# Performance work log

Hardware: AMD Instinct MI355X
Metric: run time of the kernel (lower is better)

## Reference

```python
import jax, jax.numpy as jnp
import numpy as np
from jax import lax

B, T = 64, 512
VOCAB, E = 16000, 128
USCRIPT, UE = 64, 16
F, MAX_NGRAM = 128, 5
C = 13  # num_classes


def setup_inputs() -> dict:
    key = jax.random.key(0)
    ks = jax.random.split(key, 18)
    inp = {
        "input_char": jax.random.randint(ks[0], (B, T), 0, VOCAB),
        "input_script": jax.random.randint(ks[1], (B, T), 0, USCRIPT),
        "input_mask": jnp.ones((B, T), dtype=bool),
        "char_emb": jax.random.normal(ks[2], (VOCAB, E), jnp.float32) * 0.02,
        "uscript_emb": jax.random.normal(ks[3], (USCRIPT, UE), jnp.float32) * 0.02,
        "dense_w": jax.random.normal(ks[4], (MAX_NGRAM * F + UE, C), jnp.float32) * 0.05,
        "dense_b": jnp.zeros((C,), jnp.float32),
        "trans": jax.random.normal(ks[5], (C, C), jnp.float32) * 0.1,
        "left_b": jax.random.normal(ks[6], (C,), jnp.float32) * 0.1,
        "right_b": jax.random.normal(ks[7], (C,), jnp.float32) * 0.1,
    }
    for i in range(1, MAX_NGRAM + 1):
        inp[f"conv_w{i}"] = jax.random.normal(ks[7 + i], (i, E, F), jnp.float32) * (1.0 / np.sqrt(i * E))
        inp[f"conv_b{i}"] = jnp.zeros((F,), jnp.float32)
    return inp


def _conv1d_same_relu(x, w, b):
    # x: [B,T,Cin], w: [K,Cin,Cout]
    y = lax.conv_general_dilated(x, w, window_strides=(1,), padding="SAME",
                                 dimension_numbers=("NWC", "WIO", "NWC"))
    return jax.nn.relu(y + b)


def _potentials(input_char, input_script, input_mask, char_emb, uscript_emb,
                conv_ws, conv_bs, dense_w, dense_b, left_b, right_b):
    emb = char_emb[input_char]              # [B,T,E]
    uemb = uscript_emb[input_script]        # [B,T,UE]
    feats = [_conv1d_same_relu(emb, w, b) for w, b in zip(conv_ws, conv_bs)]
    ctx = jnp.concatenate(feats + [uemb], axis=-1)          # [B,T,5F+UE]
    pot = jnp.einsum("btf,fc->btc", ctx, dense_w) + dense_b  # [B,T,C]
    # boundary energies (tfa CRF use_boundary=True): add left_b at first
    # valid step, right_b at last valid step per the mask
    m = input_mask.astype(pot.dtype)[..., None]              # [B,T,1]
    prev_m = jnp.pad(m[:, :-1], ((0, 0), (1, 0), (0, 0)))
    next_m = jnp.pad(m[:, 1:], ((0, 0), (0, 1), (0, 0)))
    pot = pot + m * (1.0 - prev_m) * left_b + m * (1.0 - next_m) * right_b
    return pot


def _viterbi_decode(pot, trans):
    # pot: [B,T,C], trans: [C,C]; full-length sequences (mask all ones)
    def fwd(state, pot_t):
        scores = state[:, :, None] + trans[None]   # [B, prev, cur]
        bp = jnp.argmax(scores, axis=1)            # [B,C]
        state = jnp.max(scores, axis=1) + pot_t    # [B,C]
        return state, bp

    final, bps = lax.scan(fwd, pot[:, 0], jnp.swapaxes(pot[:, 1:], 0, 1))
    last = jnp.argmax(final, axis=-1)              # [B]

    def back(tag, bp_t):
        prev = jnp.take_along_axis(bp_t, tag[:, None], axis=1)[:, 0]
        return prev, prev

    _, tags = lax.scan(back, last, bps, reverse=True)  # [T-1, B], forward order
    decoded = jnp.concatenate([jnp.swapaxes(tags, 0, 1), last[:, None]], axis=1)
    return decoded.astype(jnp.int32)


def reference(input_char, input_script, input_mask, char_emb, uscript_emb,
              conv_w1, conv_b1, conv_w2, conv_b2, conv_w3, conv_b3,
              conv_w4, conv_b4, conv_w5, conv_b5,
              dense_w, dense_b, trans, left_b, right_b):
    conv_ws = [conv_w1, conv_w2, conv_w3, conv_w4, conv_w5]
    conv_bs = [conv_b1, conv_b2, conv_b3, conv_b4, conv_b5]
    pot = _potentials(input_char, input_script, input_mask, char_emb, uscript_emb,
                      conv_ws, conv_bs, dense_w, dense_b, left_b, right_b)
    seq_len = jnp.sum(input_mask.astype(jnp.int32), axis=1)
    decoded = _viterbi_decode(pot, trans)
    return decoded, pot, seq_len, trans
```

## Files before the change

### kernel.cpp

```cpp
#include <hip/hip_runtime.h>

#define NB 64
#define NT 512
#define NC 13
#define AP 136
#define WP 72

typedef short s8v __attribute__((ext_vector_type(8)));
typedef float f4v __attribute__((ext_vector_type(4)));
typedef unsigned short ush;
typedef unsigned int u32;

__device__ __forceinline__ ush f2bf(float f){
    union { float f; u32 u; } v; v.f = f;
    u32 r = v.u + 0x7fffu + ((v.u >> 16) & 1u);
    return (ush)(r >> 16);
}
__device__ __forceinline__ float bf2f(ush h){
    union { u32 u; float f; } v; v.u = ((u32)h) << 16; return v.f;
}

__global__ __launch_bounds__(512)
void pot_kernel(const int* __restrict__ input_char,
                const int* __restrict__ input_script,
                const float* __restrict__ char_emb,
                const float* __restrict__ uscript_emb,
                const float* __restrict__ dense_w,
                const float* __restrict__ dense_b,
                const float* __restrict__ left_b,
                const float* __restrict__ right_b,
                const float* __restrict__ cw1, const float* __restrict__ cb1,
                const float* __restrict__ cw2, const float* __restrict__ cb2,
                const float* __restrict__ cw3, const float* __restrict__ cb3,
                const float* __restrict__ cw4, const float* __restrict__ cb4,
                const float* __restrict__ cw5, const float* __restrict__ cb5,
                float* __restrict__ out_pot)
{
    __shared__ __align__(16) ush smem[71744];
    ush* Ah     = smem;
    ush* Al     = smem + 17952;
    ush* Wh     = smem + 35904;
    ush* Wl     = smem + 45120;
    ush* feat_h = smem + 54336;
    ush* feat_l = smem + 63040;
    float* dwlds = (float*)(smem + 35904);
    float* dwue  = (float*)(smem + 39232);
    float* uebt  = (float*)(smem + 39648);

    const int tid  = threadIdx.x;
    const int lane = tid & 63;
    const int wid  = tid >> 6;
    const int tg   = wid >> 2;
    const int fg   = wid & 3;
    const int lr   = lane & 15;
    const int lq   = lane >> 4;
    const int bb   = blockIdx.x >> 2;
    const int t0   = (blockIdx.x & 3) << 7;

    for (int i = tid; i < 132*16; i += 512) {
        int row = i >> 4, s = (i & 15) << 3;
        int t = t0 + row - 2;
        uint4 hv = {0,0,0,0}, lv = {0,0,0,0};
        if (t >= 0 && t < NT) {
            int ch = input_char[bb*NT + t];
            const float* src = char_emb + ch*128 + s;
            float4 x0 = *(const float4*)src;
            float4 x1 = *(const float4*)(src + 4);
            float fs[8] = {x0.x,x0.y,x0.z,x0.w,x1.x,x1.y,x1.z,x1.w};
            ush h[8], l[8];
            #pragma unroll
            for (int q = 0; q < 8; ++q) {
                h[q] = f2bf(fs[q]);
                l[q] = f2bf(fs[q] - bf2f(h[q]));
            }
            hv.x = h[0] | ((u32)h[1]<<16); hv.y = h[2] | ((u32)h[3]<<16);
            hv.z = h[4] | ((u32)h[5]<<16); hv.w = h[6] | ((u32)h[7]<<16);
            lv.x = l[0] | ((u32)l[1]<<16); lv.y = l[2] | ((u32)l[3]<<16);
            lv.z = l[4] | ((u32)l[5]<<16); lv.w = l[6] | ((u32)l[7]<<16);
        }
        *(uint4*)&Ah[row*AP + s] = hv;
        *(uint4*)&Al[row*AP + s] = lv;
    }

    const float* cws[5] = {cw1, cw2, cw3, cw4, cw5};
    const float* cbs[5] = {cb1, cb2, cb3, cb4, cb5};

    f4v cacc[4][2];
    #pragma unroll
    for (int mt = 0; mt < 4; ++mt)
        #pragma unroll
        for (int nt = 0; nt < 2; ++nt) cacc[mt][nt] = (f4v){0.f,0.f,0.f,0.f};
    f4v dacc = (f4v){0.f,0.f,0.f,0.f};

    #pragma unroll 1
    for (int u = 0; u < 30; ++u) {
        int ut  = u >> 1, eh = u & 1;
        int fb  = ut<1?0: ut<3?1: ut<6?2: ut<10?3:4;
        int jj  = ut - fb*(fb+1)/2;
        int jsh = (2 - (fb >> 1)) + jj;
        const float* cw = cws[fb] + (jj*128 + eh*64)*128;

        __syncthreads();
        for (int g = tid; g < 1024; g += 512) {
            int f = g & 127, e8 = (g >> 7) << 3;
            float v[8];
            #pragma unroll
            for (int q = 0; q < 8; ++q) v[q] = cw[(e8 + q)*128 + f];
            ush h8[8], l8[8];
            #pragma unroll
            for (int q = 0; q < 8; ++q) {
                h8[q] = f2bf(v[q]);
                l8[q] = f2bf(v[q] - bf2f(h8[q]));
            }
            uint4 hv, lv;
            hv.x = h8[0] | ((u32)h8[1]<<16); hv.y = h8[2] | ((u32)h8[3]<<16);
            hv.z = h8[4] | ((u32)h8[5]<<16); hv.w = h8[6] | ((u32)h8[7]<<16);
            lv.x = l8[0] | ((u32)l8[1]<<16); lv.y = l8[2] | ((u32)l8[3]<<16);
            lv.z = l8[4] | ((u32)l8[5]<<16); lv.w = l8[6] | ((u32)l8[7]<<16);
            *(uint4*)&Wh[f*WP + e8] = hv;
            *(uint4*)&Wl[f*WP + e8] = lv;
        }
        __syncthreads();

        #pragma unroll
        for (int kk = 0; kk < 2; ++kk) {
            int ko = kk*32 + (lq << 3);
            s8v bh[2], bl[2];
            #pragma unroll
            for (int nt = 0; nt < 2; ++nt) {
                int frow = fg*32 + nt*16 + lr;
                bh[nt] = *(const s8v*)&Wh[frow*WP + ko];
                bl[nt] = *(const s8v*)&Wl[frow*WP + ko];
            }
            #pragma unroll
            for (int mt = 0; mt < 4; ++mt) {
                int row = tg*64 + mt*16 + lr + jsh;
                int ai  = row*AP + eh*64 + ko;
                s8v ah = *(const s8v*)&Ah[ai];
                s8v al = *(const s8v*)&Al[ai];
                #pragma unroll
                for (int nt = 0; nt < 2; ++nt) {
                    cacc[mt][nt] = __builtin_amdgcn_mfma_f32_16x16x32_bf16(ah, bh[nt], cacc[mt][nt], 0,0,0);
                    cacc[mt][nt] = __builtin_amdgcn_mfma_f32_16x16x32_bf16(ah, bl[nt], cacc[mt][nt], 0,0,0);
                    cacc[mt][nt] = __builtin_amdgcn_mfma_f32_16x16x32_bf16(al, bh[nt], cacc[mt][nt], 0,0,0);
                }
            }
        }

        if (u == 1 || u == 5 || u == 11 || u == 19 || u == 29) {
            __syncthreads();
            for (int i = tid; i < 128*13; i += 512)
                dwlds[i] = dense_w[fb*128*13 + i];
            if (fb == 4) {
                for (int i = tid; i < 16*13; i += 512)
                    dwue[i] = dense_w[640*13 + i];
                for (int i = tid; i < 2048; i += 512) {
                    int uu = i >> 7, tl = i & 127;
                    uebt[uu*128 + tl] = uscript_emb[input_script[bb*NT + t0 + tl]*16 + uu];
                }
            }
            __syncthreads();

            float cbv0 = cbs[fb][fg*32 + lr];
            float cbv1 = cbs[fb][fg*32 + 16 + lr];

            #pragma unroll 1
            for (int h = 0; h < 2; ++h) {
                if (tg == h) {
                    #pragma unroll
                    for (int mt = 0; mt < 4; ++mt)
                        #pragma unroll
                        for (int nt = 0; nt < 2; ++nt)
                            #pragma unroll
                            for (int r = 0; r < 4; ++r) {
                                float v = fmaxf(cacc[mt][nt][r] + (nt ? cbv1 : cbv0), 0.f);
                                int rw = mt*16 + (lq << 2) + r;
                                int f  = fg*32 + nt*16 + lr;
                                ush hh = f2bf(v);
                                feat_h[rw*AP + f] = hh;
                                feat_l[rw*AP + f] = f2bf(v - bf2f(hh));
                            }
                }
                __syncthreads();
                if (tg == h) {
                    int trow = fg*16 + lr;
                    #pragma unroll
                    for (int kf = 0; kf < 4; ++kf) {
                        int f0 = kf*32 + (lq << 3);
                        float dv[8];
                        #pragma unroll
                        for (int q = 0; q < 8; ++q) dv[q] = dwlds[(f0 + q)*13 + lr];
                        s8v a2h, a2l;
                        #pragma unroll
                        for (int q = 0; q < 8; ++q) {
                            ush hh = f2bf(dv[q]);
                            a2h[q] = (short)hh;
                            a2l[q] = (short)f2bf(dv[q] - bf2f(hh));
                        }
                        s8v b2h = *(const s8v*)&feat_h[trow*AP + f0];
                        s8v b2l = *(const s8v*)&feat_l[trow*AP + f0];
                        dacc = __builtin_amdgcn_mfma_f32_16x16x32_bf16(a2h, b2h, dacc, 0,0,0);
                        dacc = __builtin_amdgcn_mfma_f32_16x16x32_bf16(a2h, b2l, dacc, 0,0,0);
                        dacc = __builtin_amdgcn_mfma_f32_16x16x32_bf16(a2l, b2h, dacc, 0,0,0);
                    }
                    if (fb == 4) {
                        int tloc  = tg*64 + fg*16 + lr;
                        int tglob = t0 + tloc;
                        float pc[4];
                        #pragma unroll
                        for (int r = 0; r < 4; ++r) pc[r] = dacc[r];
                        #pragma unroll
                        for (int uu = 0; uu < 16; ++uu) {
                            float uv = uebt[uu*128 + tloc];
                            #pragma unroll
                            for (int r = 0; r < 4; ++r) {
                                int c = (lq << 2) + r;
                                if (c < 13) pc[r] = fmaf(uv, dwue[uu*13 + c], pc[r]);
                            }
                        }
                        #pragma unroll
                        for (int r = 0; r < 4; ++r) {
                            int c = (lq << 2) + r;
                            if (c < 13) {
                                float v = pc[r] + dense_b[c];
                                if (tglob == 0)    v += left_b[c];
                                if (tglob == NT-1) v += right_b[c];
                                out_pot[(bb*NT + tglob)*13 + c] = v;
                            }
                        }
                    }
                }
                __syncthreads();
            }
            #pragma unroll
            for (int mt = 0; mt < 4; ++mt)
                #pragma unroll
                for (int nt = 0; nt < 2; ++nt) cacc[mt][nt] = (f4v){0.f,0.f,0.f,0.f};
        }
    }
}

__global__ __launch_bounds__(256)
void viterbi_kernel(const float* __restrict__ pot,
                    const float* __restrict__ trans,
                    float* __restrict__ out_dec,
                    float* __restrict__ out_seq,
                    float* __restrict__ out_trans)
{
    __shared__ __align__(16) float s_lds[NT * NC];
    __shared__ float t_lds[NC * NC];
    __shared__ unsigned char path_lds[16 * 13 * 32];
    __shared__ unsigned char entry_lds[16 * 13];
    __shared__ int chunk_e[16];

    const int b   = blockIdx.x;
    const int tid = threadIdx.x;

    {
        const float4* src = reinterpret_cast<const float4*>(pot + b * NT * NC);
        float4* dst = reinterpret_cast<float4*>(s_lds);
        for (int i = tid; i < NT * NC / 4; i += 256) dst[i] = src[i];
        for (int i = tid; i < NC * NC; i += 256) t_lds[i] = trans[i];
    }
    __syncthreads();

    if (tid < 64) {
        const int c = tid;
        const bool act = c < NC;
        float tc[13];
        #pragma unroll
        for (int p = 0; p < NC; ++p) tc[p] = t_lds[p * NC + (act ? c : 0)];
        float s = act ? s_lds[c] : -1e30f;

        for (int t = 1; t < NT; ++t) {
            float v[13];
            #pragma unroll
            for (int p = 0; p < NC; ++p) v[p] = __shfl(s, p) + tc[p];
            float m0 = fmaxf(fmaxf(v[0], v[1]), fmaxf(v[2], v[3]));
            float m1 = fmaxf(fmaxf(v[4], v[5]), fmaxf(v[6], v[7]));
            float m2 = fmaxf(fmaxf(v[8], v[9]), fmaxf(v[10], v[11]));
            float best = fmaxf(fmaxf(m0, m1), fmaxf(m2, v[12]));
            float pv = act ? s_lds[t * NC + c] : 0.f;
            s = best + pv;
            if (act) s_lds[t * NC + c] = s;
        }
    }
    __syncthreads();

    if (tid < 16 * 13) {
        const int chunk = tid / 13;
        const int e     = tid - chunk * 13;
        unsigned char* path = &path_lds[(chunk * 13 + e) * 32];
        int cur = e;
        path[31] = (unsigned char)e;
        for (int tl = 31; tl >= 1; --tl) {
            const float* srow = &s_lds[(chunk * 32 + tl - 1) * NC];
            float best = -1e30f; int bi = 0;
            #pragma unroll
            for (int p = 0; p < NC; ++p) {
                float v = srow[p] + t_lds[p * NC + cur];
                if (v > best) { best = v; bi = p; }
            }
            cur = bi;
            path[tl - 1] = (unsigned char)cur;
        }
        if (chunk > 0) {
            const float* srow = &s_lds[(chunk * 32 - 1) * NC];
            float best = -1e30f; int bi = 0;
            #pragma unroll
            for (int p = 0; p < NC; ++p) {
                float v = srow[p] + t_lds[p * NC + cur];
                if (v > best) { best = v; bi = p; }
            }
            entry_lds[chunk * 13 + e] = (unsigned char)bi;
        }
    }
    __syncthreads();

    if (tid == 0) {
        float best = -1e30f; int last = 0;
        for (int c = 0; c < NC; ++c) {
            float v = s_lds[(NT - 1) * NC + c];
            if (v > best) { best = v; last = c; }
        }
        chunk_e[15] = last;
        for (int i = 15; i >= 1; --i)
            chunk_e[i - 1] = entry_lds[i * 13 + chunk_e[i]];
    }
    __syncthreads();

    float* dec = out_dec + b * NT;
    for (int t = tid; t < NT; t += 256) {
        int ck = t >> 5;
        dec[t] = (float)path_lds[(ck * 13 + chunk_e[ck]) * 32 + (t & 31)];
    }
    if (tid == 0) out_seq[b] = (float)NT;
    if (b == 0) {
        for (int i = tid; i < NC * NC; i += 256) out_trans[i] = trans[i];
    }
}

extern "C" void kernel_launch(void* const* d_in, const int* in_sizes, int n_in,
                              void* d_out, int out_size, void* d_ws, size_t ws_size,
                              hipStream_t stream) {
    const int*   input_char   = (const int*)d_in[0];
    const int*   input_script = (const int*)d_in[1];
    const float* char_emb     = (const float*)d_in[3];
    const float* uscript_emb  = (const float*)d_in[4];
    const float* dense_w      = (const float*)d_in[5];
    const float* dense_b      = (const float*)d_in[6];
    const float* trans        = (const float*)d_in[7];
    const float* left_b       = (const float*)d_in[8];
    const float* right_b      = (const float*)d_in[9];
    const float* cw1 = (const float*)d_in[10];
    const float* cb1 = (const float*)d_in[11];
    const float* cw2 = (const float*)d_in[12];
    const float* cb2 = (const float*)d_in[13];
    const float* cw3 = (const float*)d_in[14];
    const float* cb3 = (const float*)d_in[15];
    const float* cw4 = (const float*)d_in[16];
    const float* cb4 = (const float*)d_in[17];
    const float* cw5 = (const float*)d_in[18];
    const float* cb5 = (const float*)d_in[19];

    float* out       = (float*)d_out;
    float* out_dec   = out;
    float* out_pot   = out + NB * NT;
    float* out_seq   = out_pot + NB * NT * NC;
    float* out_trans = out_seq + NB;

    hipLaunchKernelGGL(pot_kernel, dim3(256), dim3(512), 0, stream,
                       input_char, input_script, char_emb, uscript_emb,
                       dense_w, dense_b, left_b, right_b,
                       cw1, cb1, cw2, cb2, cw3, cb3, cw4, cb4, cw5, cb5,
                       out_pot);

    hipLaunchKernelGGL(viterbi_kernel, dim3(NB), dim3(256), 0, stream,
                       out_pot, trans, out_dec, out_seq, out_trans);
}
```

Baseline: 191.4 us.

## Pre-split conv and dense weights into bf16 hi/lo workspace with prefetched staging

Adds a prep kernel that converts the conv weights and dense weights once into a padded bf16 hi/lo layout in the workspace. The main potentials kernel then streams each weight tile into shared memory with a plain vector copy, prefetching the next tile into registers while the current tile's MFMAs run. It also reads the dense-weight fragments directly from the workspace. This removes the per-block float-to-bf16 split and transposition of weights that all 256 blocks used to repeat. The cost is an extra kernel launch, a workspace dependency, and more register pressure from the prefetch buffer. The old kernel is kept as a fallback for when the workspace is too small.

```diff
diff --git a/kernel.cpp b/kernel.cpp
--- a/kernel.cpp
+++ b/kernel.cpp
@@ -5,6 +5,10 @@
 #define NC 13
 #define AP 136
 #define WP 72
+#define USTRIDE 18432
+#define DWT_H   552960
+#define DWT_L   563200
+#define WS_NEED 1146880
 
 typedef short s8v __attribute__((ext_vector_type(8)));
 typedef float f4v __attribute__((ext_vector_type(4)));
@@ -21,20 +25,266 @@
 }
 
 __global__ __launch_bounds__(512)
-void pot_kernel(const int* __restrict__ input_char,
-                const int* __restrict__ input_script,
-                const float* __restrict__ char_emb,
-                const float* __restrict__ uscript_emb,
-                const float* __restrict__ dense_w,
-                const float* __restrict__ dense_b,
-                const float* __restrict__ left_b,
-                const float* __restrict__ right_b,
-                const float* __restrict__ cw1, const float* __restrict__ cb1,
-                const float* __restrict__ cw2, const float* __restrict__ cb2,
-                const float* __restrict__ cw3, const float* __restrict__ cb3,
-                const float* __restrict__ cw4, const float* __restrict__ cb4,
-                const float* __restrict__ cw5, const float* __restrict__ cb5,
-                float* __restrict__ out_pot)
+void prep_kernel(const float* __restrict__ cw1, const float* __restrict__ cw2,
+                 const float* __restrict__ cw3, const float* __restrict__ cw4,
+                 const float* __restrict__ cw5, const float* __restrict__ dense_w,
+                 ush* __restrict__ ws)
+{
+    int bx = blockIdx.x, tid = threadIdx.x;
+    if (bx < 240) {
+        int u = bx >> 3, chunk = bx & 7;
+        int ut = u >> 1, eh = u & 1;
+        int fb = ut<1?0: ut<3?1: ut<6?2: ut<10?3:4;
+        int jj = ut - fb*(fb+1)/2;
+        const float* cw = fb==0?cw1: fb==1?cw2: fb==2?cw3: fb==3?cw4: cw5;
+        #pragma unroll
+        for (int q = 0; q < 2; ++q) {
+            int idx = chunk*1024 + q*512 + tid;
+            int f = idx >> 6, e = idx & 63;
+            float w = cw[(jj*128 + eh*64 + e)*128 + f];
+            ush hi = f2bf(w);
+            ws[u*USTRIDE + f*WP + e]        = hi;
+            ws[u*USTRIDE + 9216 + f*WP + e] = f2bf(w - bf2f(hi));
+        }
+    } else {
+        int fb = bx - 240;
+        #pragma unroll
+        for (int q = 0; q < 4; ++q) {
+            int idx = q*512 + tid;
+            int c = idx >> 7, f = idx & 127;
+            float v = (c < 13) ? dense_w[(fb*128 + f)*13 + c] : 0.f;
+            ush hi = f2bf(v);
+            ws[DWT_H + fb*2048 + idx] = hi;
+            ws[DWT_L + fb*2048 + idx] = f2bf(v - bf2f(hi));
+        }
+    }
+}
+
+__global__ __launch_bounds__(512)
+void pot_kernel_ws(const int* __restrict__ input_char,
+                   const int* __restrict__ input_script,
+                   const float* __restrict__ char_emb,
+                   const float* __restrict__ uscript_emb,
+                   const float* __restrict__ dense_w,
+                   const float* __restrict__ dense_b,
+                   const float* __restrict__ left_b,
+                   const float* __restrict__ right_b,
+                   const float* __restrict__ cb1, const float* __restrict__ cb2,
+                   const float* __restrict__ cb3, const float* __restrict__ cb4,
+                   const float* __restrict__ cb5,
+                   const ush* __restrict__ ws,
+                   float* __restrict__ out_pot)
+{
+    __shared__ __align__(16) ush smem[76256];
+    ush* Ah     = smem;
+    ush* Al     = smem + 17952;
+    ush* Wh     = smem + 35904;
+    ush* Wl     = smem + 45120;
+    ush* feat_h = smem + 54336;
+    ush* feat_l = smem + 63040;
+    float* uebt = (float*)(smem + 71744);
+    float* dwue = (float*)(smem + 75840);
+
+    const int tid  = threadIdx.x;
+    const int lane = tid & 63;
+    const int wid  = tid >> 6;
+    const int tg   = wid >> 2;
+    const int fg   = wid & 3;
+    const int lr   = lane & 15;
+    const int lq   = lane >> 4;
+    const int bb   = blockIdx.x >> 2;
+    const int t0   = (blockIdx.x & 3) << 7;
+
+    for (int i = tid; i < 132*16; i += 512) {
+        int row = i >> 4, s = (i & 15) << 3;
+        int t = t0 + row - 2;
+        uint4 hv = {0,0,0,0}, lv = {0,0,0,0};
+        if (t >= 0 && t < NT) {
+            int ch = input_char[bb*NT + t];
+            const float* src = char_emb + ch*128 + s;
+            float4 x0 = *(const float4*)src;
+            float4 x1 = *(const float4*)(src + 4);
+            float fs[8] = {x0.x,x0.y,x0.z,x0.w,x1.x,x1.y,x1.z,x1.w};
+            ush h[8], l[8];
+            #pragma unroll
+            for (int q = 0; q < 8; ++q) {
+                h[q] = f2bf(fs[q]);
+                l[q] = f2bf(fs[q] - bf2f(h[q]));
+            }
+            hv.x = h[0] | ((u32)h[1]<<16); hv.y = h[2] | ((u32)h[3]<<16);
+            hv.z = h[4] | ((u32)h[5]<<16); hv.w = h[6] | ((u32)h[7]<<16);
+            lv.x = l[0] | ((u32)l[1]<<16); lv.y = l[2] | ((u32)l[3]<<16);
+            lv.z = l[4] | ((u32)l[5]<<16); lv.w = l[6] | ((u32)l[7]<<16);
+        }
+        *(uint4*)&Ah[row*AP + s] = hv;
+        *(uint4*)&Al[row*AP + s] = lv;
+    }
+    for (int i = tid; i < 2048; i += 512) {
+        int uu = i >> 7, tl = i & 127;
+        uebt[uu*128 + tl] = uscript_emb[input_script[bb*NT + t0 + tl]*16 + uu];
+    }
+    if (tid < 208) dwue[tid] = dense_w[640*13 + tid];
+    {
+        const uint4* s0 = (const uint4*)ws;
+        uint4* dst = (uint4*)Wh;
+        #pragma unroll
+        for (int q = 0; q < 5; ++q) {
+            int i = tid + q*512;
+            if (i < 2304) dst[i] = s0[i];
+        }
+    }
+    __syncthreads();
+
+    const float* cbs[5] = {cb1, cb2, cb3, cb4, cb5};
+
+    f4v cacc[4][2];
+    #pragma unroll
+    for (int mt = 0; mt < 4; ++mt)
+        #pragma unroll
+        for (int nt = 0; nt < 2; ++nt) cacc[mt][nt] = (f4v){0.f,0.f,0.f,0.f};
+    f4v dacc = (f4v){0.f,0.f,0.f,0.f};
+
+    #pragma unroll 1
+    for (int u = 0; u < 30; ++u) {
+        int ut  = u >> 1, eh = u & 1;
+        int fb  = ut<1?0: ut<3?1: ut<6?2: ut<10?3:4;
+        int jj  = ut - fb*(fb+1)/2;
+        int jsh = (2 - (fb >> 1)) + jj;
+
+        uint4 pre[5];
+        if (u < 29) {
+            const uint4* src = (const uint4*)(ws + (u + 1)*USTRIDE);
+            #pragma unroll
+            for (int q = 0; q < 5; ++q) {
+                int i = tid + q*512;
+                if (i < 2304) pre[q] = src[i];
+            }
+        }
+
+        #pragma unroll
+        for (int kk = 0; kk < 2; ++kk) {
+            int ko = kk*32 + (lq << 3);
+            s8v bh[2], bl[2];
+            #pragma unroll
+            for (int nt = 0; nt < 2; ++nt) {
+                int frow = fg*32 + nt*16 + lr;
+                bh[nt] = *(const s8v*)&Wh[frow*WP + ko];
+                bl[nt] = *(const s8v*)&Wl[frow*WP + ko];
+            }
+            #pragma unroll
+            for (int mt = 0; mt < 4; ++mt) {
+                int row = tg*64 + mt*16 + lr + jsh;
+                int ai  = row*AP + eh*64 + ko;
+                s8v ah = *(const s8v*)&Ah[ai];
+                s8v al = *(const s8v*)&Al[ai];
+                #pragma unroll
+                for (int nt = 0; nt < 2; ++nt) {
+                    cacc[mt][nt] = __builtin_amdgcn_mfma_f32_16x16x32_bf16(ah, bh[nt], cacc[mt][nt], 0,0,0);
+                    cacc[mt][nt] = __builtin_amdgcn_mfma_f32_16x16x32_bf16(ah, bl[nt], cacc[mt][nt], 0,0,0);
+                    cacc[mt][nt] = __builtin_amdgcn_mfma_f32_16x16x32_bf16(al, bh[nt], cacc[mt][nt], 0,0,0);
+                }
+            }
+        }
+
+        if (u == 1 || u == 5 || u == 11 || u == 19 || u == 29) {
+            float cbv0 = cbs[fb][fg*32 + lr];
+            float cbv1 = cbs[fb][fg*32 + 16 + lr];
+
+            #pragma unroll 1
+            for (int h = 0; h < 2; ++h) {
+                if (tg == h) {
+                    #pragma unroll
+                    for (int mt = 0; mt < 4; ++mt)
+                        #pragma unroll
+                        for (int nt = 0; nt < 2; ++nt)
+                            #pragma unroll
+                            for (int r = 0; r < 4; ++r) {
+                                float v = fmaxf(cacc[mt][nt][r] + (nt ? cbv1 : cbv0), 0.f);
+                                int rw = mt*16 + (lq << 2) + r;
+                                int f  = fg*32 + nt*16 + lr;
+                                ush hh = f2bf(v);
+                                feat_h[rw*AP + f] = hh;
+                                feat_l[rw*AP + f] = f2bf(v - bf2f(hh));
+                            }
+                }
+                __syncthreads();
+                if (tg == h) {
+                    int trow = fg*16 + lr;
+                    #pragma unroll
+                    for (int kf = 0; kf < 4; ++kf) {
+                        int f0 = kf*32 + (lq << 3);
+                        s8v a2h = *(const s8v*)&ws[DWT_H + fb*2048 + lr*128 + f0];
+                        s8v a2l = *(const s8v*)&ws[DWT_L + fb*2048 + lr*128 + f0];
+                        s8v b2h = *(const s8v*)&feat_h[trow*AP + f0];
+                        s8v b2l = *(const s8v*)&feat_l[trow*AP + f0];
+                        dacc = __builtin_amdgcn_mfma_f32_16x16x32_bf16(a2h, b2h, dacc, 0,0,0);
+                        dacc = __builtin_amdgcn_mfma_f32_16x16x32_bf16(a2h, b2l, dacc, 0,0,0);
+                        dacc = __builtin_amdgcn_mfma_f32_16x16x32_bf16(a2l, b2h, dacc, 0,0,0);
+                    }
+                    if (fb == 4) {
+                        int tloc  = tg*64 + fg*16 + lr;
+                        int tglob = t0 + tloc;
+                        float pc[4];
+                        #pragma unroll
+                        for (int r = 0; r < 4; ++r) pc[r] = dacc[r];
+                        #pragma unroll
+                        for (int uu = 0; uu < 16; ++uu) {
+                            float uv = uebt[uu*128 + tloc];
+                            #pragma unroll
+                            for (int r = 0; r < 4; ++r) {
+                                int c = (lq << 2) + r;
+                                if (c < 13) pc[r] = fmaf(uv, dwue[uu*13 + c], pc[r]);
+                            }
+                        }
+                        #pragma unroll
+                        for (int r = 0; r < 4; ++r) {
+                            int c = (lq << 2) + r;
+                            if (c < 13) {
+                                float v = pc[r] + dense_b[c];
+                                if (tglob == 0)    v += left_b[c];
+                                if (tglob == NT-1) v += right_b[c];
+                                out_pot[(bb*NT + tglob)*13 + c] = v;
+                            }
+                        }
+                    }
+                }
+                __syncthreads();
+            }
+            #pragma unroll
+            for (int mt = 0; mt < 4; ++mt)
+                #pragma unroll
+                for (int nt = 0; nt < 2; ++nt) cacc[mt][nt] = (f4v){0.f,0.f,0.f,0.f};
+        } else {
+            __syncthreads();
+        }
+
+        if (u < 29) {
+            uint4* dst = (uint4*)Wh;
+            #pragma unroll
+            for (int q = 0; q < 5; ++q) {
+                int i = tid + q*512;
+                if (i < 2304) dst[i] = pre[q];
+            }
+        }
+        __syncthreads();
+    }
+}
+
+__global__ __launch_bounds__(512)
+void pot_kernel_fb(const int* __restrict__ input_char,
+                   const int* __restrict__ input_script,
+                   const float* __restrict__ char_emb,
+                   const float* __restrict__ uscript_emb,
+                   const float* __restrict__ dense_w,
+                   const float* __restrict__ dense_b,
+                   const float* __restrict__ left_b,
+                   const float* __restrict__ right_b,
+                   const float* __restrict__ cw1, const float* __restrict__ cb1,
+                   const float* __restrict__ cw2, const float* __restrict__ cb2,
+                   const float* __restrict__ cw3, const float* __restrict__ cb3,
+                   const float* __restrict__ cw4, const float* __restrict__ cb4,
+                   const float* __restrict__ cw5, const float* __restrict__ cb5,
+                   float* __restrict__ out_pot)
 {
     __shared__ __align__(16) ush smem[71744];
     ush* Ah     = smem;
@@ -369,11 +619,21 @@
     float* out_seq   = out_pot + NB * NT * NC;
     float* out_trans = out_seq + NB;
 
-    hipLaunchKernelGGL(pot_kernel, dim3(256), dim3(512), 0, stream,
-                       input_char, input_script, char_emb, uscript_emb,
-                       dense_w, dense_b, left_b, right_b,
-                       cw1, cb1, cw2, cb2, cw3, cb3, cw4, cb4, cw5, cb5,
-                       out_pot);
+    if (ws_size >= (size_t)WS_NEED) {
+        hipLaunchKernelGGL(prep_kernel, dim3(245), dim3(512), 0, stream,
+                           cw1, cw2, cw3, cw4, cw5, dense_w, (ush*)d_ws);
+        hipLaunchKernelGGL(pot_kernel_ws, dim3(256), dim3(512), 0, stream,
+                           input_char, input_script, char_emb, uscript_emb,
+                           dense_w, dense_b, left_b, right_b,
+                           cb1, cb2, cb3, cb4, cb5,
+                           (const ush*)d_ws, out_pot);
+    } else {
+        hipLaunchKernelGGL(pot_kernel_fb, dim3(256), dim3(512), 0, stream,
+                           input_char, input_script, char_emb, uscript_emb,
+                           dense_w, dense_b, left_b, right_b,
+                           cw1, cb1, cw2, cb2, cw3, cb3, cw4, cb4, cw5, cb5,
+                           out_pot);
+    }
 
     hipLaunchKernelGGL(viterbi_kernel, dim3(NB), dim3(256), 0, stream,
                        out_pot, trans, out_dec, out_seq, out_trans);
```

Measured after the change: 230.7 us. 1.21x slower.
